# Performance work log

Hardware: AMD Instinct MI355X
Metric: run time of the kernel (lower is better)

The kernel has to match this reference:

```python
import jax, jax.numpy as jnp
import numpy as np

MANTISA_BIT = 8.0  # mantisa_bit init arg


def conv3d(x, w, b, stride=1, pad=1):
    # x: [N,C,D,H,W], w: [O,I,kD,kH,kW]
    out = jax.lax.conv_general_dilated(
        x, w,
        window_strides=(stride, stride, stride),
        padding=[(pad, pad)] * 3,
        dimension_numbers=("NCDHW", "OIDHW", "NCDHW"),
    )
    return out + b.reshape(1, -1, 1, 1, 1)


def bfp_quant(x, ch_exp, m_bits):
    # Block floating point: shared per-channel exponent ch_exp [C],
    # signed mantissa with m_bits total bits. scale = 2^(m-1-exp);
    # q = clip(round(x*scale), -(2^(m-1)-1), 2^(m-1)-1)/scale
    scale = jnp.exp2(m_bits - 1.0 - ch_exp).reshape(1, -1, 1, 1, 1)
    lim = 2.0 ** (m_bits - 1.0) - 1.0
    return jnp.clip(jnp.round(x * scale), -lim, lim) / scale


def setup_inputs() -> dict:
    key = jax.random.key(0)
    ks = jax.random.split(key, 7)
    N, C_in, C_out, T, H, W, K = 8, 64, 64, 16, 56, 56, 3
    x = jax.random.normal(ks[0], (N, C_in, T, H, W), jnp.float32)
    w1 = jax.random.normal(ks[1], (C_out, C_in, K, K, K), jnp.float32) * 0.05
    b1 = jax.random.normal(ks[2], (C_out,), jnp.float32) * 0.05
    w2 = jax.random.normal(ks[3], (C_out, C_out, K, K, K), jnp.float32) * 0.05
    b2 = jax.random.normal(ks[4], (C_out,), jnp.float32) * 0.05
    # offline-optimized per-channel shared exponents (opt_exp_act_list[0], [1])
    exp1 = jax.random.randint(ks[5], (C_out,), 2, 6).astype(jnp.float32)
    exp2 = jax.random.randint(ks[6], (C_out,), 2, 6).astype(jnp.float32)
    return {"x": x, "w1": w1, "b1": b1, "w2": w2, "b2": b2,
            "exp1": exp1, "exp2": exp2}


def reference(x, w1, b1, w2, b2, exp1, exp2):
    # conv1 -> BFP quant -> ReLU
    res = conv3d(x, w1, b1)
    res = jax.nn.relu(bfp_quant(res, exp1, MANTISA_BIT))
    # conv2 -> BFP quant
    res = conv3d(res, w2, b2)
    res = bfp_quant(res, exp2, MANTISA_BIT)
    # identity shortcut (downsample=False) quantized with opt_exp_act_list[1]
    x_q = bfp_quant(x, exp2, MANTISA_BIT)
    return jax.nn.relu(x_q + res)
```

## Files before the change

kernel.cpp:

```cpp
#include <hip/hip_runtime.h>
#include <hip/hip_bf16.h>

#define Nn 8
#define Cc 64
#define Tt 16
#define Hh 56
#define Ww 56

typedef __bf16 bf16x8 __attribute__((ext_vector_type(8)));
typedef float f32x16 __attribute__((ext_vector_type(16)));
typedef unsigned short u16;
typedef unsigned int u32;

__device__ __forceinline__ u16 f32_to_bf16(float f) {
    u32 u = __float_as_uint(f);
    u32 r = (u + 0x7FFFu + ((u >> 16) & 1u)) >> 16;
    return (u16)r;
}
__device__ __forceinline__ float bf16_to_f32(u16 h) {
    return __uint_as_float(((u32)h) << 16);
}

__device__ __forceinline__ void gload16(const void* gsrc, void* lds) {
    __builtin_amdgcn_global_load_lds(
        (const __attribute__((address_space(1))) u32*)gsrc,
        (__attribute__((address_space(3))) u32*)lds, 16, 0, 0);
}

__global__ __launch_bounds__(256) void prep_w_kernel(
    const float* __restrict__ w1, const float* __restrict__ w2,
    u16* __restrict__ w1h, u16* __restrict__ w1l,
    u16* __restrict__ w2h, u16* __restrict__ w2l,
    u16* __restrict__ zpage)
{
    int idx = blockIdx.x * 256 + threadIdx.x;
    if (idx >= 221184) {
        ((uint4*)zpage)[idx - 221184] = make_uint4(0, 0, 0, 0);
        return;
    }
    int conv = idx / 110592;
    int rem  = idx % 110592;
    int tap  = rem >> 12;
    int co   = (rem >> 6) & 63;
    int ci   = rem & 63;
    const float* w = conv ? w2 : w1;
    float v = w[co * 1728 + ci * 27 + tap];
    u16 hi = f32_to_bf16(v);
    u16 lo = f32_to_bf16(v - bf16_to_f32(hi));
    int dst = tap * 4096 + co * 64 + ci;
    if (conv) { w2h[dst] = hi; w2l[dst] = lo; }
    else      { w1h[dst] = hi; w1l[dst] = lo; }
}

__global__ __launch_bounds__(256) void split_x_kernel(
    const float* __restrict__ x, u16* __restrict__ xh)
{
    __shared__ float tile[Cc][Hh + 1];
    const int tid = threadIdx.x;
    const int bid = blockIdx.x;
    const int h = bid % Hh;
    const int t = (bid / Hh) % Tt;
    const int n = bid / (Hh * Tt);
    for (int it = 0; it < 14; ++it) {
        int id = it * 256 + tid;
        int ci = id / Ww, w = id % Ww;
        tile[ci][w] = x[(((size_t)(n * Cc + ci) * Tt + t) * Hh + h) * Ww + w];
    }
    __syncthreads();
    const size_t obase = (size_t)bid * (Ww * Cc);
    for (int it = 0; it < 7; ++it) {
        int j = it * 256 + tid;
        int w = j >> 5, ci0 = (j & 31) << 1;
        u16 h0 = f32_to_bf16(tile[ci0][w]);
        u16 h1 = f32_to_bf16(tile[ci0 + 1][w]);
        *(ushort2*)(xh + obase + (size_t)w * Cc + ci0) = make_ushort2(h0, h1);
    }
}

#define SLICE_B 3712
#define A1_BUF  40960
#define B1_BUF  36864
#define C1_SMEM (A1_BUF + B1_BUF)
#define C2_BOFF 40960
#define C2_SMEM 81920

__device__ __forceinline__ const bf16x8* frag_ptr(const char* base, int row, int slot) {
    int col = (slot * 16) ^ (((row >> 1) & 3) << 4);
    return (const bf16x8*)(base + row * 64 + col);
}

__global__ __launch_bounds__(256, 2) void conv1_mfma_kernel(
    const u16* __restrict__ xh,
    const u16* __restrict__ w1h, const u16* __restrict__ w1l,
    const float* __restrict__ b1, const float* __restrict__ e1,
    const u16* __restrict__ zpage, u16* __restrict__ res1)
{
    __shared__ __align__(16) char smem[C1_SMEM];

    const int tid = threadIdx.x;
    const int l = tid & 63, wid = tid >> 6;
    const int l31 = l & 31, hi5 = l >> 5;
    const int wbase = tid & ~63;
    const int bid = (blockIdx.x & 7) * 112 + (blockIdx.x >> 3);
    const int hb = bid % 7;
    const int t  = (bid / 7) % Tt;
    const int n  = bid / (7 * Tt);
    const int h0 = hb * 8;

    f32x16 acc[2][2][2] = {};

    auto ISSUE_A = [&](int slab) {
        char* dst = smem;
        const int cih = slab / 3, kd = slab % 3;
        const int td = t + kd - 1;
        const bool tdv = (td >= 0 && td < Tt);
        const size_t tdbase = (size_t)(n * Tt + (tdv ? td : 0)) * ((size_t)Hh * Ww * Cc);
#pragma unroll
        for (int it = 0; it < 10; ++it) {
            int fi = it * 256 + tid;
            int u = fi / 232, c = fi - u * 232;
            int r = c >> 2, slot = c & 3;
            int hh = h0 - 1 + u;
            int slog = slot ^ ((r >> 1) & 3);
            const u16* src = xh + tdbase
                + ((size_t)hh * Ww + (r - 1)) * Cc + cih * 32 + slog * 8;
            bool valid = tdv & (fi < 2320) & (hh >= 0) & (hh < Hh) & (r >= 1) & (r <= Ww);
            if (!valid) src = zpage;
            gload16(src, dst + (it * 256 + wbase) * 16);
        }
    };
    auto ISSUE_B = [&](int sub) {
        char* dst = smem + A1_BUF;
        const int slab = sub >> 1, hl = sub & 1;
        const int cih = slab / 3, kd = slab % 3;
        const u16* wsrc = hl ? w1l : w1h;
#pragma unroll
        for (int it = 0; it < 9; ++it) {
            int fi = it * 256 + tid;
            int u = fi >> 8, c = fi & 255;
            int co = c >> 2, slot = c & 3;
            int slog = slot ^ ((co >> 1) & 3);
            const u16* src = wsrc + (kd * 9 + u) * 4096 + co * 64 + cih * 32 + slog * 8;
            gload16(src, dst + (it * 256 + wbase) * 16);
        }
    };

#pragma unroll 1
    for (int j = 0; j < 12; ++j) {
        __builtin_amdgcn_sched_barrier(0);
        __builtin_amdgcn_s_barrier();
        __builtin_amdgcn_sched_barrier(0);
        if ((j & 1) == 0) ISSUE_A(j >> 1);
        ISSUE_B(j);
        asm volatile("s_waitcnt vmcnt(0)" ::: "memory");
        __builtin_amdgcn_s_barrier();
        __builtin_amdgcn_sched_barrier(0);
        const char* Bcur = smem + A1_BUF;
#pragma unroll
        for (int kh = 0; kh < 3; ++kh) {
#pragma unroll
            for (int kw = 0; kw < 3; ++kw) {
                const int tap9 = kh * 3 + kw;
                bf16x8 b[2][2];
#pragma unroll
                for (int nt = 0; nt < 2; ++nt)
#pragma unroll
                    for (int kk = 0; kk < 2; ++kk)
                        b[nt][kk] = *frag_ptr(Bcur + tap9 * 4096, l31 + 32 * nt, kk * 2 + hi5);
#pragma unroll
                for (int dh = 0; dh < 2; ++dh) {
                    const char* Ak = smem + (size_t)(2 * wid + dh + kh) * SLICE_B;
                    bf16x8 a[2][2];
#pragma unroll
                    for (int m = 0; m < 2; ++m)
#pragma unroll
                        for (int kk = 0; kk < 2; ++kk)
                            a[m][kk] = *frag_ptr(Ak, l31 + 32 * m + kw, kk * 2 + hi5);
                    __builtin_amdgcn_s_setprio(1);
#pragma unroll
                    for (int m = 0; m < 2; ++m)
#pragma unroll
                        for (int nt = 0; nt < 2; ++nt)
#pragma unroll
                            for (int kk = 0; kk < 2; ++kk)
                                acc[dh][m][nt] = __builtin_amdgcn_mfma_f32_32x32x16_bf16(
                                    a[m][kk], b[nt][kk], acc[dh][m][nt], 0, 0, 0);
                    __builtin_amdgcn_s_setprio(0);
                }
            }
        }
    }

#pragma unroll
    for (int dh = 0; dh < 2; ++dh) {
        const int h = h0 + 2 * wid + dh;
        const size_t rowbase = ((size_t)(n * Tt + t) * Hh + h) * ((size_t)Ww * Cc);
#pragma unroll
        for (int nt = 0; nt < 2; ++nt) {
            int co = 32 * nt + l31;
            float e = e1[co];
            float sc = exp2f(7.0f - e), inv = exp2f(e - 7.0f);
            float bias = b1[co];
#pragma unroll
            for (int m = 0; m < 2; ++m)
#pragma unroll
                for (int reg = 0; reg < 16; ++reg) {
                    int w = 32 * m + (reg & 3) + 8 * (reg >> 2) + 4 * hi5;
                    if (w < Ww) {
                        float v = acc[dh][m][nt][reg] + bias;
                        float q = rintf(v * sc);
                        q = fminf(fmaxf(q, -127.f), 127.f);
                        v = fmaxf(q * inv, 0.0f);
                        res1[rowbase + (size_t)w * Cc + co] = f32_to_bf16(v);
                    }
                }
        }
    }
}

__global__ __launch_bounds__(256, 2) void conv2_mfma_kernel(
    const u16* __restrict__ a, const u16* __restrict__ w2h,
    const float* __restrict__ b2, const float* __restrict__ e2,
    const float* __restrict__ x, const u16* __restrict__ zpage,
    float* __restrict__ out)
{
    __shared__ __align__(16) char smem[C2_SMEM];
    char* As = smem;
    char* Bs = smem + C2_BOFF;

    const int tid = threadIdx.x;
    const int l = tid & 63, wid = tid >> 6;
    const int l31 = l & 31, hi5 = l >> 5;
    const int wbase = tid & ~63;
    const int bid = (blockIdx.x & 7) * 112 + (blockIdx.x >> 3);
    const int hb = bid % 7;
    const int t  = (bid / 7) % Tt;
    const int n  = bid / (7 * Tt);
    const int h0 = hb * 8;

    f32x16 acc[2][2][2] = {};

#pragma unroll 1
    for (int cih = 0; cih < 2; ++cih) {
#pragma unroll 1
      for (int kd = 0; kd < 3; ++kd) {
        const int td = t + kd - 1;
        if (td < 0 || td >= Tt) continue;
        __builtin_amdgcn_sched_barrier(0);
        __builtin_amdgcn_s_barrier();
        __builtin_amdgcn_sched_barrier(0);
        {
          const size_t tdbase = (size_t)(n * Tt + td) * ((size_t)Hh * Ww * Cc);
#pragma unroll
          for (int it = 0; it < 10; ++it) {
            int fi = it * 256 + tid;
            int u = fi / 232, c = fi - u * 232;
            int r = c >> 2, slot = c & 3;
            int hh = h0 - 1 + u;
            int slog = slot ^ ((r >> 1) & 3);
            const u16* src = a + tdbase
                + ((size_t)hh * Ww + (r - 1)) * Cc + cih * 32 + slog * 8;
            bool valid = (fi < 2320) & (hh >= 0) & (hh < Hh) & (r >= 1) & (r <= Ww);
            if (!valid) src = zpage;
            gload16(src, As + (it * 256 + wbase) * 16);
          }
        }
        {
#pragma unroll
          for (int it = 0; it < 9; ++it) {
            int fi = it * 256 + tid;
            int u = fi >> 8, c = fi & 255;
            int co = c >> 2, slot = c & 3;
            int slog = slot ^ ((co >> 1) & 3);
            const u16* src = w2h + (kd * 9 + u) * 4096 + co * 64 + cih * 32 + slog * 8;
            gload16(src, Bs + (it * 256 + wbase) * 16);
          }
        }
        asm volatile("s_waitcnt vmcnt(0)" ::: "memory");
        __builtin_amdgcn_s_barrier();
        __builtin_amdgcn_sched_barrier(0);
#pragma unroll
        for (int kh = 0; kh < 3; ++kh) {
#pragma unroll
          for (int kw = 0; kw < 3; ++kw) {
            const int tap9 = kh * 3 + kw;
            bf16x8 b[2][2];
#pragma unroll
            for (int nt = 0; nt < 2; ++nt)
#pragma unroll
              for (int kk = 0; kk < 2; ++kk)
                b[nt][kk] = *frag_ptr(Bs + tap9 * 4096, l31 + 32 * nt, kk * 2 + hi5);
#pragma unroll
            for (int dh = 0; dh < 2; ++dh) {
              const char* Ak = As + (size_t)(2 * wid + dh + kh) * SLICE_B;
              bf16x8 a2[2][2];
#pragma unroll
              for (int m = 0; m < 2; ++m)
#pragma unroll
                for (int kk = 0; kk < 2; ++kk)
                  a2[m][kk] = *frag_ptr(Ak, l31 + 32 * m + kw, kk * 2 + hi5);
              __builtin_amdgcn_s_setprio(1);
#pragma unroll
              for (int m = 0; m < 2; ++m)
#pragma unroll
                for (int nt = 0; nt < 2; ++nt)
#pragma unroll
                  for (int kk = 0; kk < 2; ++kk)
                    acc[dh][m][nt] = __builtin_amdgcn_mfma_f32_32x32x16_bf16(
                        a2[m][kk], b[nt][kk], acc[dh][m][nt], 0, 0, 0);
              __builtin_amdgcn_s_setprio(0);
            }
          }
        }
      }
    }
#pragma unroll
    for (int dh = 0; dh < 2; ++dh) {
      const int h = h0 + 2 * wid + dh;
#pragma unroll
      for (int nt = 0; nt < 2; ++nt) {
        int co = 32 * nt + l31;
        float e = e2[co];
        float sc = exp2f(7.0f - e), inv = exp2f(e - 7.0f);
        float bias = b2[co];
#pragma unroll
        for (int m = 0; m < 2; ++m)
#pragma unroll
          for (int reg = 0; reg < 16; ++reg) {
            int w = 32 * m + (reg & 3) + 8 * (reg >> 2) + 4 * hi5;
            if (w < Ww) {
              float v = acc[dh][m][nt][reg] + bias;
              float q = rintf(v * sc);
              q = fminf(fmaxf(q, -127.f), 127.f);
              v = q * inv;
              size_t xi = (((size_t)(n * Cc + co) * Tt + t) * Hh + h) * Ww + w;
              float xv = x[xi];
              float qx = rintf(xv * sc);
              qx = fminf(fmaxf(qx, -127.f), 127.f);
              out[xi] = fmaxf(qx * inv + v, 0.0f);
            }
          }
      }
    }
}

extern "C" void kernel_launch(void* const* d_in, const int* in_sizes, int n_in,
                              void* d_out, int out_size, void* d_ws, size_t ws_size,
                              hipStream_t stream) {
    const float* x  = (const float*)d_in[0];
    const float* w1 = (const float*)d_in[1];
    const float* b1 = (const float*)d_in[2];
    const float* w2 = (const float*)d_in[3];
    const float* b2 = (const float*)d_in[4];
    const float* e1 = (const float*)d_in[5];
    const float* e2 = (const float*)d_in[6];

    u16* xh = (u16*)d_out;
    char* ws = (char*)d_ws;
    u16* w1h = (u16*)(ws);
    u16* w1l = (u16*)(ws + 221184);
    u16* w2h = (u16*)(ws + 442368);
    u16* w2l = (u16*)(ws + 663552);
    u16* zpage = (u16*)(ws + 884736);
    u16* res1  = (u16*)(ws + 888832);

    prep_w_kernel<<<865, 256, 0, stream>>>(w1, w2, w1h, w1l, w2h, w2l, zpage);
    split_x_kernel<<<Nn * Tt * Hh, 256, 0, stream>>>(x, xh);
    conv1_mfma_kernel<<<896, 256, 0, stream>>>(xh, w1h, w1l, b1, e1, zpage, res1);
    conv2_mfma_kernel<<<896, 256, 0, stream>>>(res1, w2h, b2, e2, x, zpage, (float*)d_out);
}
```

Baseline: 334.8 us.

## Double-buffer weight chunks per kh to overlap weight loads with MFMA

Both conv kernels now split the weight slab into per-kh chunks of three taps, held in two small LDS buffers. The next chunk is prefetched while the current one is consumed, using a partial vmcnt wait. This is meant to hide global-to-LDS weight load latency behind MFMA work and to cut LDS use, which may allow more occupancy. In exchange it adds more barriers per iteration, A-slab loads are still not double-buffered, and conv2 no longer skips out-of-range depth slices; it zero-fills them and computes on them instead.

```diff
diff --git a/kernel.cpp b/kernel.cpp
--- a/kernel.cpp
+++ b/kernel.cpp
@@ -79,10 +79,9 @@
 
 #define SLICE_B 3712
 #define A1_BUF  40960
-#define B1_BUF  36864
-#define C1_SMEM (A1_BUF + B1_BUF)
-#define C2_BOFF 40960
-#define C2_SMEM 81920
+#define BC_BUF  12288
+#define C1_SMEM (A1_BUF + 2 * BC_BUF)
+#define C2_SMEM (A1_BUF + 2 * BC_BUF)
 
 __device__ __forceinline__ const bf16x8* frag_ptr(const char* base, int row, int slot) {
     int col = (slot * 16) ^ (((row >> 1) & 3) << 4);
@@ -129,66 +128,70 @@
             gload16(src, dst + (it * 256 + wbase) * 16);
         }
     };
-    auto ISSUE_B = [&](int sub) {
-        char* dst = smem + A1_BUF;
-        const int slab = sub >> 1, hl = sub & 1;
+    auto ISSUE_B = [&](int ch) {
+        char* dst = smem + A1_BUF + (ch & 1) * BC_BUF;
+        const int slab = ch / 6, sub = ch % 6;
+        const int hl = sub / 3, kh = sub % 3;
         const int cih = slab / 3, kd = slab % 3;
         const u16* wsrc = hl ? w1l : w1h;
 #pragma unroll
-        for (int it = 0; it < 9; ++it) {
+        for (int it = 0; it < 3; ++it) {
             int fi = it * 256 + tid;
             int u = fi >> 8, c = fi & 255;
             int co = c >> 2, slot = c & 3;
             int slog = slot ^ ((co >> 1) & 3);
-            const u16* src = wsrc + (kd * 9 + u) * 4096 + co * 64 + cih * 32 + slog * 8;
+            const u16* src = wsrc + ((kd * 3 + kh) * 3 + u) * 4096
+                + co * 64 + cih * 32 + slog * 8;
             gload16(src, dst + (it * 256 + wbase) * 16);
         }
     };
 
+    ISSUE_A(0);
+    ISSUE_B(0);
+
 #pragma unroll 1
-    for (int j = 0; j < 12; ++j) {
-        __builtin_amdgcn_sched_barrier(0);
+    for (int ch = 0; ch < 36; ++ch) {
+        if (ch > 0 && (ch % 6) == 0) ISSUE_A(ch / 6);
+        if (ch < 35) ISSUE_B(ch + 1);
+        __builtin_amdgcn_sched_barrier(0);
+        if (ch == 35) { asm volatile("s_waitcnt vmcnt(0)" ::: "memory"); }
+        else          { asm volatile("s_waitcnt vmcnt(3)" ::: "memory"); }
         __builtin_amdgcn_s_barrier();
         __builtin_amdgcn_sched_barrier(0);
-        if ((j & 1) == 0) ISSUE_A(j >> 1);
-        ISSUE_B(j);
-        asm volatile("s_waitcnt vmcnt(0)" ::: "memory");
+        const int kh = ch % 3;
+        const char* Bc = smem + A1_BUF + (ch & 1) * BC_BUF;
+#pragma unroll
+        for (int kw = 0; kw < 3; ++kw) {
+            bf16x8 b[2][2];
+#pragma unroll
+            for (int nt = 0; nt < 2; ++nt)
+#pragma unroll
+                for (int kk = 0; kk < 2; ++kk)
+                    b[nt][kk] = *frag_ptr(Bc + kw * 4096, l31 + 32 * nt, kk * 2 + hi5);
+#pragma unroll
+            for (int dh = 0; dh < 2; ++dh) {
+                const char* Ak = smem + (size_t)(2 * wid + dh + kh) * SLICE_B;
+                bf16x8 a[2][2];
+#pragma unroll
+                for (int m = 0; m < 2; ++m)
+#pragma unroll
+                    for (int kk = 0; kk < 2; ++kk)
+                        a[m][kk] = *frag_ptr(Ak, l31 + 32 * m + kw, kk * 2 + hi5);
+                __builtin_amdgcn_s_setprio(1);
+#pragma unroll
+                for (int m = 0; m < 2; ++m)
+#pragma unroll
+                    for (int nt = 0; nt < 2; ++nt)
+#pragma unroll
+                        for (int kk = 0; kk < 2; ++kk)
+                            acc[dh][m][nt] = __builtin_amdgcn_mfma_f32_32x32x16_bf16(
+                                a[m][kk], b[nt][kk], acc[dh][m][nt], 0, 0, 0);
+                __builtin_amdgcn_s_setprio(0);
+            }
+        }
+        __builtin_amdgcn_sched_barrier(0);
         __builtin_amdgcn_s_barrier();
         __builtin_amdgcn_sched_barrier(0);
-        const char* Bcur = smem + A1_BUF;
-#pragma unroll
-        for (int kh = 0; kh < 3; ++kh) {
-#pragma unroll
-            for (int kw = 0; kw < 3; ++kw) {
-                const int tap9 = kh * 3 + kw;
-                bf16x8 b[2][2];
-#pragma unroll
-                for (int nt = 0; nt < 2; ++nt)
-#pragma unroll
-                    for (int kk = 0; kk < 2; ++kk)
-                        b[nt][kk] = *frag_ptr(Bcur + tap9 * 4096, l31 + 32 * nt, kk * 2 + hi5);
-#pragma unroll
-                for (int dh = 0; dh < 2; ++dh) {
-                    const char* Ak = smem + (size_t)(2 * wid + dh + kh) * SLICE_B;
-                    bf16x8 a[2][2];
-#pragma unroll
-                    for (int m = 0; m < 2; ++m)
-#pragma unroll
-                        for (int kk = 0; kk < 2; ++kk)
-                            a[m][kk] = *frag_ptr(Ak, l31 + 32 * m + kw, kk * 2 + hi5);
-                    __builtin_amdgcn_s_setprio(1);
-#pragma unroll
-                    for (int m = 0; m < 2; ++m)
-#pragma unroll
-                        for (int nt = 0; nt < 2; ++nt)
-#pragma unroll
-                            for (int kk = 0; kk < 2; ++kk)
-                                acc[dh][m][nt] = __builtin_amdgcn_mfma_f32_32x32x16_bf16(
-                                    a[m][kk], b[nt][kk], acc[dh][m][nt], 0, 0, 0);
-                    __builtin_amdgcn_s_setprio(0);
-                }
-            }
-        }
     }
 
 #pragma unroll
@@ -225,8 +228,6 @@
     float* __restrict__ out)
 {
     __shared__ __align__(16) char smem[C2_SMEM];
-    char* As = smem;
-    char* Bs = smem + C2_BOFF;
 
     const int tid = threadIdx.x;
     const int l = tid & 63, wid = tid >> 6;
@@ -240,19 +241,14 @@
 
     f32x16 acc[2][2][2] = {};
 
-#pragma unroll 1
-    for (int cih = 0; cih < 2; ++cih) {
-#pragma unroll 1
-      for (int kd = 0; kd < 3; ++kd) {
+    auto ISSUE_A = [&](int slab) {
+        char* dst = smem;
+        const int cih = slab / 3, kd = slab % 3;
         const int td = t + kd - 1;
-        if (td < 0 || td >= Tt) continue;
-        __builtin_amdgcn_sched_barrier(0);
-        __builtin_amdgcn_s_barrier();
-        __builtin_amdgcn_sched_barrier(0);
-        {
-          const size_t tdbase = (size_t)(n * Tt + td) * ((size_t)Hh * Ww * Cc);
-#pragma unroll
-          for (int it = 0; it < 10; ++it) {
+        const bool tdv = (td >= 0 && td < Tt);
+        const size_t tdbase = (size_t)(n * Tt + (tdv ? td : 0)) * ((size_t)Hh * Ww * Cc);
+#pragma unroll
+        for (int it = 0; it < 10; ++it) {
             int fi = it * 256 + tid;
             int u = fi / 232, c = fi - u * 232;
             int r = c >> 2, slot = c & 3;
@@ -260,60 +256,75 @@
             int slog = slot ^ ((r >> 1) & 3);
             const u16* src = a + tdbase
                 + ((size_t)hh * Ww + (r - 1)) * Cc + cih * 32 + slog * 8;
-            bool valid = (fi < 2320) & (hh >= 0) & (hh < Hh) & (r >= 1) & (r <= Ww);
+            bool valid = tdv & (fi < 2320) & (hh >= 0) & (hh < Hh) & (r >= 1) & (r <= Ww);
             if (!valid) src = zpage;
-            gload16(src, As + (it * 256 + wbase) * 16);
-          }
-        }
-        {
-#pragma unroll
-          for (int it = 0; it < 9; ++it) {
+            gload16(src, dst + (it * 256 + wbase) * 16);
+        }
+    };
+    auto ISSUE_B = [&](int ch) {
+        char* dst = smem + A1_BUF + (ch & 1) * BC_BUF;
+        const int slab = ch / 3, kh = ch % 3;
+        const int cih = slab / 3, kd = slab % 3;
+#pragma unroll
+        for (int it = 0; it < 3; ++it) {
             int fi = it * 256 + tid;
             int u = fi >> 8, c = fi & 255;
             int co = c >> 2, slot = c & 3;
             int slog = slot ^ ((co >> 1) & 3);
-            const u16* src = w2h + (kd * 9 + u) * 4096 + co * 64 + cih * 32 + slog * 8;
-            gload16(src, Bs + (it * 256 + wbase) * 16);
-          }
-        }
-        asm volatile("s_waitcnt vmcnt(0)" ::: "memory");
+            const u16* src = w2h + ((kd * 3 + kh) * 3 + u) * 4096
+                + co * 64 + cih * 32 + slog * 8;
+            gload16(src, dst + (it * 256 + wbase) * 16);
+        }
+    };
+
+    ISSUE_A(0);
+    ISSUE_B(0);
+
+#pragma unroll 1
+    for (int ch = 0; ch < 18; ++ch) {
+        if (ch > 0 && (ch % 3) == 0) ISSUE_A(ch / 3);
+        if (ch < 17) ISSUE_B(ch + 1);
+        __builtin_amdgcn_sched_barrier(0);
+        if (ch == 17) { asm volatile("s_waitcnt vmcnt(0)" ::: "memory"); }
+        else          { asm volatile("s_waitcnt vmcnt(3)" ::: "memory"); }
         __builtin_amdgcn_s_barrier();
         __builtin_amdgcn_sched_barrier(0);
-#pragma unroll
-        for (int kh = 0; kh < 3; ++kh) {
-#pragma unroll
-          for (int kw = 0; kw < 3; ++kw) {
-            const int tap9 = kh * 3 + kw;
+        const int kh = ch % 3;
+        const char* Bc = smem + A1_BUF + (ch & 1) * BC_BUF;
+#pragma unroll
+        for (int kw = 0; kw < 3; ++kw) {
             bf16x8 b[2][2];
 #pragma unroll
             for (int nt = 0; nt < 2; ++nt)
 #pragma unroll
-              for (int kk = 0; kk < 2; ++kk)
-                b[nt][kk] = *frag_ptr(Bs + tap9 * 4096, l31 + 32 * nt, kk * 2 + hi5);
+                for (int kk = 0; kk < 2; ++kk)
+                    b[nt][kk] = *frag_ptr(Bc + kw * 4096, l31 + 32 * nt, kk * 2 + hi5);
 #pragma unroll
             for (int dh = 0; dh < 2; ++dh) {
-              const char* Ak = As + (size_t)(2 * wid + dh + kh) * SLICE_B;
-              bf16x8 a2[2][2];
-#pragma unroll
-              for (int m = 0; m < 2; ++m)
-#pragma unroll
-                for (int kk = 0; kk < 2; ++kk)
-                  a2[m][kk] = *frag_ptr(Ak, l31 + 32 * m + kw, kk * 2 + hi5);
-              __builtin_amdgcn_s_setprio(1);
-#pragma unroll
-              for (int m = 0; m < 2; ++m)
-#pragma unroll
-                for (int nt = 0; nt < 2; ++nt)
-#pragma unroll
-                  for (int kk = 0; kk < 2; ++kk)
-                    acc[dh][m][nt] = __builtin_amdgcn_mfma_f32_32x32x16_bf16(
-                        a2[m][kk], b[nt][kk], acc[dh][m][nt], 0, 0, 0);
-              __builtin_amdgcn_s_setprio(0);
+                const char* Ak = smem + (size_t)(2 * wid + dh + kh) * SLICE_B;
+                bf16x8 a2[2][2];
+#pragma unroll
+                for (int m = 0; m < 2; ++m)
+#pragma unroll
+                    for (int kk = 0; kk < 2; ++kk)
+                        a2[m][kk] = *frag_ptr(Ak, l31 + 32 * m + kw, kk * 2 + hi5);
+                __builtin_amdgcn_s_setprio(1);
+#pragma unroll
+                for (int m = 0; m < 2; ++m)
+#pragma unroll
+                    for (int nt = 0; nt < 2; ++nt)
+#pragma unroll
+                        for (int kk = 0; kk < 2; ++kk)
+                            acc[dh][m][nt] = __builtin_amdgcn_mfma_f32_32x32x16_bf16(
+                                a2[m][kk], b[nt][kk], acc[dh][m][nt], 0, 0, 0);
+                __builtin_amdgcn_s_setprio(0);
             }
-          }
-        }
-      }
-    }
+        }
+        __builtin_amdgcn_sched_barrier(0);
+        __builtin_amdgcn_s_barrier();
+        __builtin_amdgcn_sched_barrier(0);
+    }
+
 #pragma unroll
     for (int dh = 0; dh < 2; ++dh) {
       const int h = h0 + 2 * wid + dh;
```

Measured after the change: 344.4 us. 1.03x slower.

## Restage conv1 weight chunks per kh row with hi/lo halves together

Applied to the files above, without the earlier changes.

The conv1 K-loop now stages the hi and lo bf16 weight splits of one kh row (3 kw taps each) in a single chunk, instead of staging all 9 taps of one split at a time. Each A fragment is read once and reused for both the hi and lo MFMAs, which halves A-fragment LDS reads. The B buffer shrinks from 36 KB to 24 KB, freeing LDS. The cost is 18 barrier/load iterations instead of 12, each with less compute, which exposes more synchronisation and load latency per iteration.

```diff
diff --git a/kernel.cpp b/kernel.cpp
--- a/kernel.cpp
+++ b/kernel.cpp
@@ -79,7 +79,7 @@
 
 #define SLICE_B 3712
 #define A1_BUF  40960
-#define B1_BUF  36864
+#define B1_BUF  24576
 #define C1_SMEM (A1_BUF + B1_BUF)
 #define C2_BOFF 40960
 #define C2_SMEM 81920
@@ -129,64 +129,72 @@
             gload16(src, dst + (it * 256 + wbase) * 16);
         }
     };
-    auto ISSUE_B = [&](int sub) {
+    auto ISSUE_B = [&](int ch) {
         char* dst = smem + A1_BUF;
-        const int slab = sub >> 1, hl = sub & 1;
+        const int slab = ch / 3, kh = ch % 3;
         const int cih = slab / 3, kd = slab % 3;
-        const u16* wsrc = hl ? w1l : w1h;
-#pragma unroll
-        for (int it = 0; it < 9; ++it) {
+#pragma unroll
+        for (int it = 0; it < 6; ++it) {
             int fi = it * 256 + tid;
             int u = fi >> 8, c = fi & 255;
             int co = c >> 2, slot = c & 3;
             int slog = slot ^ ((co >> 1) & 3);
-            const u16* src = wsrc + (kd * 9 + u) * 4096 + co * 64 + cih * 32 + slog * 8;
+            int hl = u / 3, kw = u % 3;
+            const u16* src = (hl ? w1l : w1h) + ((kd * 3 + kh) * 3 + kw) * 4096
+                + co * 64 + cih * 32 + slog * 8;
             gload16(src, dst + (it * 256 + wbase) * 16);
         }
     };
 
 #pragma unroll 1
-    for (int j = 0; j < 12; ++j) {
+    for (int ch = 0; ch < 18; ++ch) {
         __builtin_amdgcn_sched_barrier(0);
         __builtin_amdgcn_s_barrier();
         __builtin_amdgcn_sched_barrier(0);
-        if ((j & 1) == 0) ISSUE_A(j >> 1);
-        ISSUE_B(j);
+        if ((ch % 3) == 0) ISSUE_A(ch / 3);
+        ISSUE_B(ch);
         asm volatile("s_waitcnt vmcnt(0)" ::: "memory");
         __builtin_amdgcn_s_barrier();
         __builtin_amdgcn_sched_barrier(0);
-        const char* Bcur = smem + A1_BUF;
-#pragma unroll
-        for (int kh = 0; kh < 3; ++kh) {
-#pragma unroll
-            for (int kw = 0; kw < 3; ++kw) {
-                const int tap9 = kh * 3 + kw;
-                bf16x8 b[2][2];
-#pragma unroll
-                for (int nt = 0; nt < 2; ++nt)
+        const int kh = ch % 3;
+        const char* Bs = smem + A1_BUF;
+#pragma unroll
+        for (int kw = 0; kw < 3; ++kw) {
+            bf16x8 bh[2][2], bl[2][2];
+#pragma unroll
+            for (int nt = 0; nt < 2; ++nt)
+#pragma unroll
+                for (int kk = 0; kk < 2; ++kk) {
+                    bh[nt][kk] = *frag_ptr(Bs + kw * 4096, l31 + 32 * nt, kk * 2 + hi5);
+                    bl[nt][kk] = *frag_ptr(Bs + 12288 + kw * 4096, l31 + 32 * nt, kk * 2 + hi5);
+                }
+#pragma unroll
+            for (int dh = 0; dh < 2; ++dh) {
+                const char* Ak = smem + (size_t)(2 * wid + dh + kh) * SLICE_B;
+                bf16x8 a[2][2];
+#pragma unroll
+                for (int m = 0; m < 2; ++m)
 #pragma unroll
                     for (int kk = 0; kk < 2; ++kk)
-                        b[nt][kk] = *frag_ptr(Bcur + tap9 * 4096, l31 + 32 * nt, kk * 2 + hi5);
-#pragma unroll
-                for (int dh = 0; dh < 2; ++dh) {
-                    const char* Ak = smem + (size_t)(2 * wid + dh + kh) * SLICE_B;
-                    bf16x8 a[2][2];
-#pragma unroll
-                    for (int m = 0; m < 2; ++m)
+                        a[m][kk] = *frag_ptr(Ak, l31 + 32 * m + kw, kk * 2 + hi5);
+                __builtin_amdgcn_s_setprio(1);
+#pragma unroll
+                for (int m = 0; m < 2; ++m)
+#pragma unroll
+                    for (int nt = 0; nt < 2; ++nt)
 #pragma unroll
                         for (int kk = 0; kk < 2; ++kk)
-                            a[m][kk] = *frag_ptr(Ak, l31 + 32 * m + kw, kk * 2 + hi5);
-                    __builtin_amdgcn_s_setprio(1);
-#pragma unroll
-                    for (int m = 0; m < 2; ++m)
-#pragma unroll
-                        for (int nt = 0; nt < 2; ++nt)
-#pragma unroll
-                            for (int kk = 0; kk < 2; ++kk)
-                                acc[dh][m][nt] = __builtin_amdgcn_mfma_f32_32x32x16_bf16(
-                                    a[m][kk], b[nt][kk], acc[dh][m][nt], 0, 0, 0);
-                    __builtin_amdgcn_s_setprio(0);
-                }
+                            acc[dh][m][nt] = __builtin_amdgcn_mfma_f32_32x32x16_bf16(
+                                a[m][kk], bh[nt][kk], acc[dh][m][nt], 0, 0, 0);
+#pragma unroll
+                for (int m = 0; m < 2; ++m)
+#pragma unroll
+                    for (int nt = 0; nt < 2; ++nt)
+#pragma unroll
+                        for (int kk = 0; kk < 2; ++kk)
+                            acc[dh][m][nt] = __builtin_amdgcn_mfma_f32_32x32x16_bf16(
+                                a[m][kk], bl[nt][kk], acc[dh][m][nt], 0, 0, 0);
+                __builtin_amdgcn_s_setprio(0);
             }
         }
     }
```

Result: no change. 335.3 us (+0.2%).
